# Kernel optimization log

Measured on AMD Instinct MI355X. Metric: run time of the kernel, lower is better.

Reference implementation:

```python
import jax, jax.numpy as jnp
import numpy as np

MAX_SAMPLES = 400  # init max_samples
EPS = 1e-9


def setup_inputs() -> dict:
    key = jax.random.key(0)
    k1, k2, k3, k4 = jax.random.split(key, 4)
    E, N, K, L = 8192, 2048, 8, 16
    # per-edge probabilities (positive, as the loss takes log of ratios)
    probas = jax.random.uniform(k1, (E,), jnp.float32, minval=1e-3, maxval=1.0)
    # soft cluster assignments: row-normalized so Bhattacharyya coeff <= 1
    c = jax.random.uniform(k2, (N, K), jnp.float32)
    clusters = c / c.sum(axis=1, keepdims=True)
    edges_nn = jax.random.randint(k3, (E, 2), 0, N)
    label_keypoints = jax.random.randint(k4, (L,), 0, N)
    return {"probas": probas, "clusters": clusters,
            "edges_nn": edges_nn, "label_keypoints": label_keypoints}


def reference(probas, clusters, edges_nn, label_keypoints):
    E = edges_nn.shape[0]
    clst = jnp.argmax(clusters, axis=1)                      # [N] hard assignment
    c0 = clst[edges_nn[:, 0]]                                # [E]
    c1 = clst[edges_nn[:, 1]]                                # [E]
    assigned = clst[label_keypoints]                         # [L] clusters at keypoints
    # edge selected if either endpoint lies in a keypoint cluster (union over labels,
    # static-shape mask form of get_edges_on_location)
    sel = jnp.any((c0[None, :] == assigned[:, None]) |
                  (c1[None, :] == assigned[:, None]), axis=0)  # [E]
    sims = c0 == c1
    pos = sel & sims                                          # positive edges
    neg = sel & ~sims                                         # negative edges
    # Bhattacharyya coefficient per edge: sum_k sqrt(p_k * q_k)
    bc = jnp.sqrt(clusters[edges_nn[:, 0]] * clusters[edges_nn[:, 1]]).sum(axis=1)  # [E]
    # pos x neg cross product, restricted to pairs sharing the anchor node edges[.,0]
    same_anchor = edges_nn[:, 0][:, None] == edges_nn[None, :, 0]   # [E,E]
    valid = pos[:, None] & neg[None, :] & same_anchor               # [E,E]
    w = 1.0 - 0.5 * (bc[:, None] + bc[None, :])                     # [E,E] sampling prob
    logw = jnp.where(valid & (w > 0),
                     jnp.log(jnp.maximum(w, EPS)), -jnp.inf)
    # multinomial-without-replacement via Gumbel top-k (deterministic key)
    u = jax.random.uniform(jax.random.key(42), (E, E), jnp.float32)
    gumbel = -jnp.log(-jnp.log(u + EPS) + EPS)
    vals, flat_idx = jax.lax.top_k((logw + gumbel).reshape(-1), MAX_SAMPLES)
    i_ = flat_idx // E                                        # positive-edge rows
    j_ = flat_idx % E                                         # negative-edge rows
    p_pos = probas[i_]
    p_neg = probas[j_]
    term = jnp.log(p_pos / (p_pos + p_neg))                   # [max_samples]
    # guard against < max_samples valid pairs (torch would just sample fewer)
    ok = jnp.isfinite(vals)
    loss = -jnp.sum(jnp.where(ok, term, 0.0)) / jnp.maximum(jnp.sum(ok), 1)
    return loss
```

## Files before the change

### kernel.cpp

```cpp
#include <hip/hip_runtime.h>
#include <stdint.h>


#define E_CONST 8192
#define N_CONST 2048
#define K_CONST 8
#define L_CONST 16
#define MAXS 400
#define EPS_F 1e-9f
#define NTHR 1024
#define RCAP 4096

#define OFF_CLUA   0
#define OFF_CLUB   32768
#define OFF_PK     65536
#define OFF_Q      73728
#define OFF_CUR    81920
#define OFF_CSR    90112
#define OFF_EDGE   106496
#define OFF_CLST   139264
#define OFF_TMP    141312
#define OFF_HIST   141376
#define OFF_WSUM   142400
#define OFF_WCNT   142464
#define OFF_MISC   142528
#define LDS_BYTES  142592

struct Cand { float val; uint32_t pack; };

__device__ __forceinline__ uint2 threefry2x32_42(uint32_t x0, uint32_t x1) {
    const uint32_t ks0 = 0u, ks1 = 42u;
    const uint32_t ks2 = ks0 ^ ks1 ^ 0x1BD11BDAu;
    const uint32_t ks[3] = {ks0, ks1, ks2};
    const int R[2][4] = {{13, 15, 26, 6}, {17, 29, 16, 24}};
    x0 += ks0; x1 += ks1;
#pragma unroll
    for (int g = 0; g < 5; ++g) {
        const int* r = R[g & 1];
#pragma unroll
        for (int q = 0; q < 4; ++q) {
            x0 += x1;
            x1 = (x1 << r[q]) | (x1 >> (32 - r[q]));
            x1 ^= x0;
        }
        x0 += ks[(g + 1) % 3];
        x1 += ks[(g + 2) % 3] + (uint32_t)(g + 1);
    }
    return make_uint2(x0, x1);
}

__device__ __forceinline__ float gumbel_at(uint32_t idx) {
    uint2 o = threefry2x32_42(0u, idx);
    uint32_t bits = o.x ^ o.y;
    float u = __uint_as_float((bits >> 9) | 0x3F800000u) - 1.0f;
    return -logf(-logf(u + EPS_F) + EPS_F);
}

__device__ __forceinline__ uint32_t sortable_key(float f) {
    uint32_t b = __float_as_uint(f);
    return (b & 0x80000000u) ? ~b : (b | 0x80000000u);
}

__device__ __forceinline__ int argmax8(float4 a, float4 b) {
    float v[8] = {a.x, a.y, a.z, a.w, b.x, b.y, b.z, b.w};
    float best = v[0]; int bi = 0;
#pragma unroll
    for (int k = 1; k < 8; ++k)
        if (v[k] > best) { best = v[k]; bi = k; }
    return bi;
}

__device__ __forceinline__ void scan_inplace(int* arr, int* tmp, int* totalOut) {
    int tid = threadIdx.x;
    int lane = tid & 63, wid = tid >> 6;
    int i0 = 2 * tid, i1 = i0 + 1;
    int v0 = arr[i0], v1 = arr[i1];
    int s = v0 + v1;
    int inc = s;
#pragma unroll
    for (int off = 1; off < 64; off <<= 1) {
        int u = __shfl_up(inc, off);
        if (lane >= off) inc += u;
    }
    if (lane == 63) tmp[wid] = inc;
    __syncthreads();
    if (wid == 0) {
        int w = (lane < 16) ? tmp[lane] : 0;
        int incw = w;
#pragma unroll
        for (int off = 1; off < 16; off <<= 1) {
            int u = __shfl_up(incw, off);
            if (lane >= off) incw += u;
        }
        if (lane < 16) tmp[lane] = incw - w;
    }
    __syncthreads();
    int base = tmp[wid] + (inc - s);
    arr[i0] = base;
    arr[i1] = base + v0;
    if (tid == 1023) *totalOut = base + v0 + v1;
    __syncthreads();
}

__global__ __launch_bounds__(1024) void k_all(
    const float* __restrict__ probas, const float* __restrict__ clusters,
    const int* __restrict__ edges, const int* __restrict__ keypts,
    Cand* __restrict__ spill, int pmax, float* __restrict__ out) {

    extern __shared__ char smem[];
    float4*   s_cluA = (float4*)(smem + OFF_CLUA);
    float4*   s_cluB = (float4*)(smem + OFF_CLUB);
    int*      s_pk   = (int*)(smem + OFF_PK);
    int*      s_q    = (int*)(smem + OFF_Q);
    int*      s_cur  = (int*)(smem + OFF_CUR);
    uint16_t* s_csr  = (uint16_t*)(smem + OFF_CSR);
    uint32_t* s_edge = (uint32_t*)(smem + OFF_EDGE);
    uint8_t*  s_clst = (uint8_t*)(smem + OFF_CLST);
    int*      s_tmp  = (int*)(smem + OFF_TMP);
    int*      s_hist = (int*)(smem + OFF_HIST);
    float*    s_wsum = (float*)(smem + OFF_WSUM);
    int*      s_wcnt = (int*)(smem + OFF_WCNT);
    int*      s_misc = (int*)(smem + OFF_MISC);

    int tid = threadIdx.x;
    s_pk[tid] = 0; s_pk[tid + 1024] = 0;
    if (tid == 0) s_misc[0] = 0;

    const float4* c4 = (const float4*)clusters;
#pragma unroll
    for (int r = 0; r < 2; ++r) {
        int n = tid + r * 1024;
        float4 a = c4[2 * n], b = c4[2 * n + 1];
        s_cluA[n] = a; s_cluB[n] = b;
        s_clst[n] = (uint8_t)argmax8(a, b);
    }
    __syncthreads();
    if (tid < L_CONST)
        atomicOr((uint32_t*)&s_misc[0], 1u << s_clst[keypts[tid]]);
    __syncthreads();
    uint32_t m = (uint32_t)s_misc[0];

    const int2* ed2 = (const int2*)edges;
    uint32_t af[8];
#pragma unroll
    for (int it = 0; it < 8; ++it) {
        int e = tid + it * NTHR;
        int2 p = ed2[e];
        s_edge[e] = ((uint32_t)p.x << 16) | (uint32_t)p.y;
        int c0 = s_clst[p.x], c1 = s_clst[p.y];
        int f = 0;
        if ((((m >> c0) | (m >> c1)) & 1u)) f = (c0 == c1) ? 1 : 2;
        af[it] = ((uint32_t)p.x << 2) | (uint32_t)f;
        if (f == 1)      atomicAdd(&s_pk[p.x], 1);
        else if (f == 2) atomicAdd(&s_pk[p.x], 0x10000);
    }
    __syncthreads();

    {
        int i0 = 2 * tid, i1 = i0 + 1;
        int p0 = s_pk[i0], p1 = s_pk[i1];
        s_q[i0] = (p0 & 0xFFFF) * (p0 >> 16);
        s_q[i1] = (p1 & 0xFFFF) * (p1 >> 16);
    }
    __syncthreads();
    scan_inplace(s_pk, s_tmp, &s_misc[1]);
    scan_inplace(s_q, s_tmp, &s_misc[2]);
    s_cur[2 * tid] = s_pk[2 * tid];
    s_cur[2 * tid + 1] = s_pk[2 * tid + 1];
    __syncthreads();
    int nPosTot = s_misc[1] & 0xFFFF;
    int nNegTot = s_misc[1] >> 16;
    int P = s_misc[2]; if (P > pmax) P = pmax;

#pragma unroll
    for (int it = 0; it < 8; ++it) {
        int f = (int)(af[it] & 3u);
        int a = (int)(af[it] >> 2);
        int e = tid + it * NTHR;
        if (f == 1) {
            int old = atomicAdd(&s_cur[a], 1);
            s_csr[old & 0xFFFF] = (uint16_t)e;
        } else if (f == 2) {
            int old = atomicAdd(&s_cur[a], 0x10000);
            s_csr[nPosTot + (old >> 16)] = (uint16_t)e;
        }
    }
    __syncthreads();

    auto bc_of = [&](int e) -> float {
        uint32_t pe = s_edge[e];
        int n0 = (int)(pe >> 16), n1 = (int)(pe & 0xFFFFu);
        float4 a0 = s_cluA[n0], a1 = s_cluB[n0];
        float4 b0 = s_cluA[n1], b1 = s_cluB[n1];
        float s = sqrtf(a0.x * b0.x);
        s += sqrtf(a0.y * b0.y);
        s += sqrtf(a0.z * b0.z);
        s += sqrtf(a0.w * b0.w);
        s += sqrtf(a1.x * b1.x);
        s += sqrtf(a1.y * b1.y);
        s += sqrtf(a1.z * b1.z);
        s += sqrtf(a1.w * b1.w);
        return s;
    };
    auto make_cand = [&](int t, float& val, uint32_t& pack) {
        int lo = 0, hi = N_CONST - 1;
#pragma unroll
        for (int itr = 0; itr < 11; ++itr) {
            int mid = (lo + hi + 1) >> 1;
            if (s_q[mid] <= t) lo = mid; else hi = mid - 1;
        }
        int a = lo;
        int loc = t - s_q[a];
        int pk = s_pk[a];
        int pb = pk & 0xFFFF, nb = pk >> 16;
        int nextN = (a < N_CONST - 1) ? (s_pk[a + 1] >> 16) : nNegTot;
        int nn = nextN - nb;
        int ip = loc / nn;
        int jn = loc - ip * nn;
        int i = s_csr[pb + ip];
        int j = s_csr[nPosTot + nb + jn];
        float w = 1.0f - 0.5f * (bc_of(i) + bc_of(j));
        val = (w > 0.0f)
            ? logf(fmaxf(w, EPS_F)) + gumbel_at((uint32_t)i * E_CONST + (uint32_t)j)
            : -INFINITY;
        pack = ((uint32_t)i << 16) | (uint32_t)j;
    };

    float vval0 = 0.f, vval1 = 0.f, vval2 = 0.f, vval3 = 0.f;
    uint32_t vpk0 = 0, vpk1 = 0, vpk2 = 0, vpk3 = 0;
    if (tid        < P) make_cand(tid,        vval0, vpk0);
    if (tid + 1024 < P) make_cand(tid + 1024, vval1, vpk1);
    if (tid + 2048 < P) make_cand(tid + 2048, vval2, vpk2);
    if (tid + 3072 < P) make_cand(tid + 3072, vval3, vpk3);
    for (int t = tid + RCAP; t < P; t += NTHR) {
        float v; uint32_t pk;
        make_cand(t, v, pk);
        spill[t - RCAP].val = v; spill[t - RCAP].pack = pk;
    }
    uint32_t vk0 = sortable_key(vval0), vk1 = sortable_key(vval1);
    uint32_t vk2 = sortable_key(vval2), vk3 = sortable_key(vval3);
    __syncthreads();

    uint32_t* s_prefix = (uint32_t*)&s_misc[3];
    int*      s_target = &s_misc[4];
    int M = P;
    uint32_t thr = 0;
    if (M > MAXS) {
        if (tid == 0) { *s_prefix = 0; *s_target = MAXS; }
        __syncthreads();
        for (int pass = 0; pass < 4; ++pass) {
            int shift = 24 - 8 * pass;
            if (tid < 256) s_hist[tid] = 0;
            __syncthreads();
            uint32_t pfx = *s_prefix;
            if (tid        < M && (pass == 0 || (vk0 >> (shift + 8)) == pfx)) atomicAdd(&s_hist[(vk0 >> shift) & 255], 1);
            if (tid + 1024 < M && (pass == 0 || (vk1 >> (shift + 8)) == pfx)) atomicAdd(&s_hist[(vk1 >> shift) & 255], 1);
            if (tid + 2048 < M && (pass == 0 || (vk2 >> (shift + 8)) == pfx)) atomicAdd(&s_hist[(vk2 >> shift) & 255], 1);
            if (tid + 3072 < M && (pass == 0 || (vk3 >> (shift + 8)) == pfx)) atomicAdd(&s_hist[(vk3 >> shift) & 255], 1);
            for (int t = tid + RCAP; t < M; t += NTHR) {
                uint32_t k = sortable_key(spill[t - RCAP].val);
                if (pass == 0 || (k >> (shift + 8)) == pfx)
                    atomicAdd(&s_hist[(k >> shift) & 255], 1);
            }
            __syncthreads();
            if (tid < 64) {
                int h0 = s_hist[4 * tid], h1 = s_hist[4 * tid + 1];
                int h2 = s_hist[4 * tid + 2], h3 = s_hist[4 * tid + 3];
                int sincl = h0 + h1 + h2 + h3;
#pragma unroll
                for (int off = 1; off < 64; off <<= 1) {
                    int v = __shfl_down(sincl, off);
                    if (tid + off < 64) sincl += v;
                }
                int excl = __shfl_down(sincl, 1);
                if (tid == 63) excl = 0;
                int suf3 = excl + h3;
                int suf2 = suf3 + h2;
                int suf1 = suf2 + h1;
                int suf0 = suf1 + h0;
                int tgt = *s_target;
                uint32_t pfxOld = *s_prefix;
                if      (suf0 >= tgt && suf1 < tgt) { *s_prefix = (pfxOld << 8) | (4u*tid+0); *s_target = tgt - suf1; }
                else if (suf1 >= tgt && suf2 < tgt) { *s_prefix = (pfxOld << 8) | (4u*tid+1); *s_target = tgt - suf2; }
                else if (suf2 >= tgt && suf3 < tgt) { *s_prefix = (pfxOld << 8) | (4u*tid+2); *s_target = tgt - suf3; }
                else if (suf3 >= tgt && excl < tgt) { *s_prefix = (pfxOld << 8) | (4u*tid+3); *s_target = tgt - excl; }
            }
            __syncthreads();
        }
        thr = *s_prefix;
    }

    float mysum = 0.f;
    int myc = 0;
    auto accum = [&](int t, float v, uint32_t k, uint32_t pk) {
        if (t < M && v != -INFINITY && k >= thr) {
            int i = (int)(pk >> 16), j = (int)(pk & 0xFFFFu);
            float pi = probas[i], pj = probas[j];
            mysum += logf(pi / (pi + pj));
            myc++;
        }
    };
    accum(tid,        vval0, vk0, vpk0);
    accum(tid + 1024, vval1, vk1, vpk1);
    accum(tid + 2048, vval2, vk2, vpk2);
    accum(tid + 3072, vval3, vk3, vpk3);
    for (int t = tid + RCAP; t < M; t += NTHR) {
        Cand c = spill[t - RCAP];
        accum(t, c.val, sortable_key(c.val), c.pack);
    }
#pragma unroll
    for (int off = 32; off > 0; off >>= 1) {
        mysum += __shfl_down(mysum, off);
        myc   += __shfl_down(myc, off);
    }
    int wid = tid >> 6;
    if ((tid & 63) == 0) { s_wsum[wid] = mysum; s_wcnt[wid] = myc; }
    __syncthreads();
    if (tid == 0) {
        float s = 0.f; int c = 0;
        for (int w = 0; w < 16; ++w) { s += s_wsum[w]; c += s_wcnt[w]; }
        if (c < 1) c = 1;
        out[0] = -s / (float)c;
    }
}

extern "C" void kernel_launch(void* const* d_in, const int* in_sizes, int n_in,
                              void* d_out, int out_size, void* d_ws, size_t ws_size,
                              hipStream_t stream) {
    const float* probas   = (const float*)d_in[0];
    const float* clusters = (const float*)d_in[1];
    const int*   edges    = (const int*)d_in[2];
    const int*   keypts   = (const int*)d_in[3];
    float* out = (float*)d_out;

    Cand* spill = (Cand*)d_ws;
    int spill_cap = (int)(ws_size / sizeof(Cand));
    if (spill_cap > 61440) spill_cap = 61440;
    int pmax = RCAP + spill_cap;

    hipFuncSetAttribute((const void*)k_all,
                        hipFuncAttributeMaxDynamicSharedMemorySize, LDS_BYTES);

    k_all<<<1, NTHR, LDS_BYTES, stream>>>(probas, clusters, edges, keypts,
                                          spill, pmax, out);
}
```

Measured before the change: 28.62 us.

## Use fast log/sqrt intrinsics, prefetch edges, and warp-aggregate histogram atomics

Replaces logf and sqrtf with the hardware fast intrinsics __logf and __builtin_amdgcn_sqrtf. Hoists the edge loads to the top of the kernel so their latency overlaps the cluster loads and argmax. Rewrites the radix-select histogram update so lanes with the same bin are found by ballot matching and only one leader per bin does the shared-memory atomic. The fast math can change the Gumbel-perturbed keys slightly, which risks altering top-k selection at ties, and the 9-step ballot match adds fixed cost per update.

```diff
diff --git a/kernel.cpp b/kernel.cpp
--- a/kernel.cpp
+++ b/kernel.cpp
@@ -53,7 +53,7 @@
     uint2 o = threefry2x32_42(0u, idx);
     uint32_t bits = o.x ^ o.y;
     float u = __uint_as_float((bits >> 9) | 0x3F800000u) - 1.0f;
-    return -logf(-logf(u + EPS_F) + EPS_F);
+    return -__logf(-__logf(u + EPS_F) + EPS_F);
 }
 
 __device__ __forceinline__ uint32_t sortable_key(float f) {
@@ -123,6 +123,13 @@
     int*      s_misc = (int*)(smem + OFF_MISC);
 
     int tid = threadIdx.x;
+    int lane = tid & 63;
+
+    const int2* ed2 = (const int2*)edges;
+    int2 pre[8];
+#pragma unroll
+    for (int it = 0; it < 8; ++it) pre[it] = ed2[tid + it * NTHR];
+
     s_pk[tid] = 0; s_pk[tid + 1024] = 0;
     if (tid == 0) s_misc[0] = 0;
 
@@ -140,12 +147,11 @@
     __syncthreads();
     uint32_t m = (uint32_t)s_misc[0];
 
-    const int2* ed2 = (const int2*)edges;
     uint32_t af[8];
 #pragma unroll
     for (int it = 0; it < 8; ++it) {
         int e = tid + it * NTHR;
-        int2 p = ed2[e];
+        int2 p = pre[it];
         s_edge[e] = ((uint32_t)p.x << 16) | (uint32_t)p.y;
         int c0 = s_clst[p.x], c1 = s_clst[p.y];
         int f = 0;
@@ -192,14 +198,14 @@
         int n0 = (int)(pe >> 16), n1 = (int)(pe & 0xFFFFu);
         float4 a0 = s_cluA[n0], a1 = s_cluB[n0];
         float4 b0 = s_cluA[n1], b1 = s_cluB[n1];
-        float s = sqrtf(a0.x * b0.x);
-        s += sqrtf(a0.y * b0.y);
-        s += sqrtf(a0.z * b0.z);
-        s += sqrtf(a0.w * b0.w);
-        s += sqrtf(a1.x * b1.x);
-        s += sqrtf(a1.y * b1.y);
-        s += sqrtf(a1.z * b1.z);
-        s += sqrtf(a1.w * b1.w);
+        float s = __builtin_amdgcn_sqrtf(a0.x * b0.x);
+        s += __builtin_amdgcn_sqrtf(a0.y * b0.y);
+        s += __builtin_amdgcn_sqrtf(a0.z * b0.z);
+        s += __builtin_amdgcn_sqrtf(a0.w * b0.w);
+        s += __builtin_amdgcn_sqrtf(a1.x * b1.x);
+        s += __builtin_amdgcn_sqrtf(a1.y * b1.y);
+        s += __builtin_amdgcn_sqrtf(a1.z * b1.z);
+        s += __builtin_amdgcn_sqrtf(a1.w * b1.w);
         return s;
     };
     auto make_cand = [&](int t, float& val, uint32_t& pack) {
@@ -221,7 +227,7 @@
         int j = s_csr[nPosTot + nb + jn];
         float w = 1.0f - 0.5f * (bc_of(i) + bc_of(j));
         val = (w > 0.0f)
-            ? logf(fmaxf(w, EPS_F)) + gumbel_at((uint32_t)i * E_CONST + (uint32_t)j)
+            ? __logf(fmaxf(w, EPS_F)) + gumbel_at((uint32_t)i * E_CONST + (uint32_t)j)
             : -INFINITY;
         pack = ((uint32_t)i << 16) | (uint32_t)j;
     };
@@ -253,10 +259,25 @@
             if (tid < 256) s_hist[tid] = 0;
             __syncthreads();
             uint32_t pfx = *s_prefix;
-            if (tid        < M && (pass == 0 || (vk0 >> (shift + 8)) == pfx)) atomicAdd(&s_hist[(vk0 >> shift) & 255], 1);
-            if (tid + 1024 < M && (pass == 0 || (vk1 >> (shift + 8)) == pfx)) atomicAdd(&s_hist[(vk1 >> shift) & 255], 1);
-            if (tid + 2048 < M && (pass == 0 || (vk2 >> (shift + 8)) == pfx)) atomicAdd(&s_hist[(vk2 >> shift) & 255], 1);
-            if (tid + 3072 < M && (pass == 0 || (vk3 >> (shift + 8)) == pfx)) atomicAdd(&s_hist[(vk3 >> shift) & 255], 1);
+            auto hist_add = [&](bool inRange, uint32_t k) {
+                bool act = inRange && (pass == 0 || (k >> (shift + 8)) == pfx);
+                uint32_t b = (k >> shift) & 255u;
+                uint32_t v = act ? b : 256u;
+                uint64_t peers = ~0ull;
+#pragma unroll
+                for (int bit = 0; bit < 9; ++bit) {
+                    uint64_t vote = __ballot((v >> bit) & 1u);
+                    peers &= ((v >> bit) & 1u) ? vote : ~vote;
+                }
+                if (act) {
+                    int leader = __ffsll((unsigned long long)peers) - 1;
+                    if (lane == leader) atomicAdd(&s_hist[b], (int)__popcll(peers));
+                }
+            };
+            hist_add(tid        < M, vk0);
+            hist_add(tid + 1024 < M, vk1);
+            hist_add(tid + 2048 < M, vk2);
+            hist_add(tid + 3072 < M, vk3);
             for (int t = tid + RCAP; t < M; t += NTHR) {
                 uint32_t k = sortable_key(spill[t - RCAP].val);
                 if (pass == 0 || (k >> (shift + 8)) == pfx)
@@ -296,7 +317,7 @@
         if (t < M && v != -INFINITY && k >= thr) {
             int i = (int)(pk >> 16), j = (int)(pk & 0xFFFFu);
             float pi = probas[i], pj = probas[j];
-            mysum += logf(pi / (pi + pj));
+            mysum += __logf(pi / (pi + pj));
             myc++;
         }
     };
```

Measured after the change: 28.00 us. 1.02x faster.
